# Performance work log

Measured on AMD Instinct MI355X. Metric: run time of the kernel, lower is better.

The kernel has to match this reference:

```python
import jax, jax.numpy as jnp
import numpy as np

MUL = 32            # multiplicity of 0e and 1o irreps
IN_DIM = MUL * 4    # 32 scalars + 32 vectors = 128
SH_DIM = 4          # 1x0e + 1x1o
N_EDGE_FEAT = 128
HIDDEN = 128
W_NUMEL = 4 * MUL * MUL  # 4 CG paths, uvw weights 32x1x32 each
EPS = 1e-5
INV_SQRT3 = 1.0 / np.sqrt(3.0)
PATH_NORM = 1.0 / np.sqrt(2.0 * MUL)  # 2 paths per output irrep, fan-in MUL


def _fc(edge_attr, W1, b1, W2, b2):
    h = jax.nn.relu(edge_attr @ W1 + b1)
    return h @ W2 + b2  # [E, W_NUMEL]


def _tensor_product(x, sh, w):
    # FullyConnectedTensorProduct for (32x0e+32x1o) x (1x0e+1x1o) -> (32x0e+32x1o)
    # CG (real w3j): 0x0->0: 1 ; 0x1->1, 1x0->1, 1x1->0: delta/sqrt(3)
    E = x.shape[0]
    x0 = x[:, :MUL]                      # [E,32]   scalars
    x1 = x[:, MUL:].reshape(E, MUL, 3)   # [E,32,3] vectors
    sh0 = sh[:, 0]                       # [E]
    sh1 = sh[:, 1:4]                     # [E,3]
    wA = w[:, 0 * MUL * MUL:1 * MUL * MUL].reshape(E, MUL, MUL)  # 0e x 0e -> 0e
    wB = w[:, 1 * MUL * MUL:2 * MUL * MUL].reshape(E, MUL, MUL)  # 0e x 1o -> 1o
    wC = w[:, 2 * MUL * MUL:3 * MUL * MUL].reshape(E, MUL, MUL)  # 1o x 0e -> 1o
    wD = w[:, 3 * MUL * MUL:4 * MUL * MUL].reshape(E, MUL, MUL)  # 1o x 1o -> 0e
    out0 = PATH_NORM * (
        jnp.einsum('eu,euw->ew', x0 * sh0[:, None], wA)
        + INV_SQRT3 * jnp.einsum('eui,ei,euw->ew', x1, sh1, wD))
    out1 = PATH_NORM * INV_SQRT3 * (
        jnp.einsum('eu,ei,euw->ewi', x0, sh1, wB)
        + jnp.einsum('eui,euw->ewi', x1 * sh0[:, None, None], wC))
    return jnp.concatenate([out0, out1.reshape(E, MUL * 3)], axis=-1)  # [E,128]


def _batch_norm(x, bn_weight, bn_bias):
    # e3nn-style equivariant BatchNorm (training stats): scalars get mean/var
    # normalization + affine; vectors get norm normalization + scale.
    N = x.shape[0]
    s = x[:, :MUL]                       # [N,32]
    v = x[:, MUL:].reshape(N, MUL, 3)    # [N,32,3]
    s = s - s.mean(axis=0)
    s = s * (jax.lax.rsqrt((s ** 2).mean(axis=0) + EPS) * bn_weight[:MUL]) + bn_bias
    v_norm = jax.lax.rsqrt((v ** 2).mean(axis=-1).mean(axis=0) + EPS)  # [32]
    v = v * (v_norm * bn_weight[MUL:])[None, :, None]
    return jnp.concatenate([s, v.reshape(N, MUL * 3)], axis=-1)


def _forward(node_attr, edge_index, edge_attr, edge_sh,
             W1, b1, W2, b2, bn_weight, bn_bias):
    edge_src, edge_dst = edge_index[0], edge_index[1]
    N = node_attr.shape[0]
    w = _fc(edge_attr, W1, b1, W2, b2)                     # [E, 4096]
    tp = _tensor_product(node_attr[edge_dst], edge_sh, w)  # [E, 128]
    # scatter mean over edge_src
    summed = jax.ops.segment_sum(tp, edge_src, num_segments=N)
    counts = jax.ops.segment_sum(jnp.ones((tp.shape[0],), tp.dtype), edge_src,
                                 num_segments=N)
    out = summed / jnp.maximum(counts, 1.0)[:, None]
    out = out + node_attr                                  # residual (same dim, pad=0)
    return _batch_norm(out, bn_weight, bn_bias)


def setup_inputs() -> dict:
    key = jax.random.key(0)
    ks = jax.random.split(key, 10)
    N, E = 10000, 60000
    node_attr = jax.random.normal(ks[0], (N, IN_DIM), jnp.float32)
    edge_index = jax.random.randint(ks[1], (2, E), 0, N)
    edge_attr = jax.random.normal(ks[2], (E, N_EDGE_FEAT), jnp.float32)
    edge_sh = jax.random.normal(ks[3], (E, SH_DIM), jnp.float32)
    W1 = jax.random.normal(ks[4], (N_EDGE_FEAT, HIDDEN), jnp.float32) / np.sqrt(N_EDGE_FEAT)
    b1 = jnp.zeros((HIDDEN,), jnp.float32)
    W2 = jax.random.normal(ks[5], (HIDDEN, W_NUMEL), jnp.float32) / np.sqrt(HIDDEN)
    b2 = jnp.zeros((W_NUMEL,), jnp.float32)
    bn_weight = jnp.ones((2 * MUL,), jnp.float32)
    bn_bias = jnp.zeros((MUL,), jnp.float32)
    return {"node_attr": node_attr, "edge_index": edge_index,
            "edge_attr": edge_attr, "edge_sh": edge_sh,
            "W1": W1, "b1": b1, "W2": W2, "b2": b2,
            "bn_weight": bn_weight, "bn_bias": bn_bias}


def reference(node_attr, edge_index, edge_attr, edge_sh,
              W1, b1, W2, b2, bn_weight, bn_bias):
    return _forward(node_attr, edge_index, edge_attr, edge_sh,
                    W1, b1, W2, b2, bn_weight, bn_bias)
```

## Files before the change

kernel.cpp:

```cpp
#include <hip/hip_runtime.h>
#include <math.h>

#define EPSV 1e-5f
#define IS3  0.57735026918962576f
#define PNRM 0.125f

typedef __attribute__((ext_vector_type(8)))  short  short8;
typedef __attribute__((ext_vector_type(16))) float  floatx16;

static __device__ inline unsigned short f2bf(float f) {
    unsigned int u = __float_as_uint(f);
    return (unsigned short)((u + 0x7fff + ((u >> 16) & 1)) >> 16);
}
static __device__ inline float bflo(unsigned int u) { return __uint_as_float(u << 16); }
static __device__ inline float bfhi(unsigned int u) { return __uint_as_float(u & 0xffff0000u); }

#define GLD16(gp, lp) __builtin_amdgcn_global_load_lds( \
    (const __attribute__((address_space(1))) unsigned int*)(gp), \
    (__attribute__((address_space(3))) unsigned int*)(lp), 16, 0, 0)

__global__ __launch_bounds__(256) void k0_sw(const float* __restrict__ src,
                                             unsigned short* __restrict__ dst,
                                             int total, int ncShift, int ncMask) {
    int i = blockIdx.x * 256 + threadIdx.x;
    if (i >= total) return;
    int k = i >> ncShift, c = i & ncMask;
    dst[(size_t)(c >> 5) * 4096 + (k >> 3) * 256 + (c & 31) * 8 + (k & 7)] = f2bf(src[i]);
}

__global__ __launch_bounds__(256) void k1_fc(const float* __restrict__ ea,
                                             const unsigned short* __restrict__ W1T,
                                             const float* __restrict__ b1,
                                             const int* __restrict__ ei,
                                             unsigned short* __restrict__ h,
                                             int* __restrict__ deg, int E) {
    __shared__ __align__(16) unsigned short W1s[16384];
    const int tid = threadIdx.x, lane = tid & 63, wv = tid >> 6;
    const int half = lane >> 5, col = lane & 31;
    const int e0 = blockIdx.x * 128;

    if (tid < 128) { int e = e0 + tid; if (e < E) atomicAdd(&deg[ei[e]], 1); }

#pragma unroll
    for (int q = 0; q < 8; ++q) {
        int chunk = wv * 8 + q;
        GLD16((const char*)W1T + chunk * 1024 + lane * 16, (char*)W1s + chunk * 1024);
    }

    int e = e0 + wv * 32 + col; if (e >= E) e = E - 1;
    short8 afr[8];
#pragma unroll
    for (int c = 0; c < 8; ++c) {
        const float4* p = (const float4*)(ea + (size_t)e * 128 + c * 16 + half * 8);
        float4 f0 = p[0], f1 = p[1];
        short8 v;
        v[0] = (short)f2bf(f0.x); v[1] = (short)f2bf(f0.y);
        v[2] = (short)f2bf(f0.z); v[3] = (short)f2bf(f0.w);
        v[4] = (short)f2bf(f1.x); v[5] = (short)f2bf(f1.y);
        v[6] = (short)f2bf(f1.z); v[7] = (short)f2bf(f1.w);
        afr[c] = v;
    }
    __syncthreads();

#pragma unroll
    for (int jt = 0; jt < 4; ++jt) {
        floatx16 d = {0,0,0,0,0,0,0,0,0,0,0,0,0,0,0,0};
#pragma unroll
        for (int c = 0; c < 8; ++c) {
            short8 bf = *(const short8*)((const char*)W1s + jt * 8192 + (2 * c + half) * 512 + col * 16);
            d = __builtin_amdgcn_mfma_f32_32x32x16_bf16(afr[c], bf, d, 0, 0, 0);
        }
        int j = jt * 32 + col;
        float b1v = b1[j];
#pragma unroll
        for (int reg = 0; reg < 16; ++reg) {
            int r = (reg & 3) + 8 * (reg >> 2) + 4 * half;
            int er = e0 + wv * 32 + r;
            if (er < E) {
                float v = d[reg] + b1v;
                v = v > 0.f ? v : 0.f;
                h[(size_t)er * 128 + j] = f2bf(v);
            }
        }
    }
}

__global__ __launch_bounds__(256, 2) void k2_mfma(const unsigned short* __restrict__ h,
                                                  const unsigned short* __restrict__ W2T,
                                                  const float* __restrict__ b2,
                                                  const float* __restrict__ na,
                                                  const int* __restrict__ ei,
                                                  const float* __restrict__ sh,
                                                  float* __restrict__ tp, int E) {
    __shared__ __align__(16) char smem[74752];
    unsigned short* As  = (unsigned short*)smem;
    unsigned short* Bs0 = (unsigned short*)(smem + 16384);
    unsigned short* Bs1 = (unsigned short*)(smem + 32768);
    unsigned short* Ctb = (unsigned short*)(smem + 49152);
    float* shs = (float*)(smem + 73728);
    float* red = (float*)smem;

    const int tid = threadIdx.x, lane = tid & 63, wv = tid >> 6;
    const int half = lane >> 5, col = lane & 31;
    const int ust = wv >> 1, esub = wv & 1;
    const int e0 = blockIdx.x * 64;

    if (tid < 64) {
        int e = e0 + tid; int ec = e < E ? e : E - 1;
        float4 s = *(const float4*)(sh + (size_t)ec * 4);
        *(float4*)&shs[tid * 4] = s;
    }

    for (int idx = tid; idx < 2048; idx += 256) {
        int el = idx & 63, u = idx >> 6;
        int e = e0 + el; int ec = e < E ? e : E - 1;
        int dn = ei[E + ec];
        const float* nar = na + (size_t)dn * 128;
        float x0  = nar[u];
        float x10 = nar[32 + u * 3], x11 = nar[33 + u * 3], x12 = nar[34 + u * 3];
        const float* shr = sh + (size_t)ec * 4;
        float s0 = shr[0], s1 = shr[1], s2 = shr[2], s3 = shr[3];
        int o = u * 64 + el;
        Ctb[0 * 2048 + o] = f2bf(x0 * s0);
        Ctb[1 * 2048 + o] = f2bf(x0);
        Ctb[2 * 2048 + o] = f2bf(x10);
        Ctb[3 * 2048 + o] = f2bf(x11);
        Ctb[4 * 2048 + o] = f2bf(x12);
        Ctb[5 * 2048 + o] = f2bf(IS3 * (x10 * s1 + x11 * s2 + x12 * s3));
    }

#pragma unroll
    for (int q = 0; q < 4; ++q) {
        int t = wv * 4 + q;
        int g = t >> 3;
        int jj = (t & 7) * 64 + lane;
        int e = e0 + g * 32 + (jj & 31); int ec = e < E ? e : E - 1;
        GLD16((const char*)h + (size_t)ec * 256 + (jj >> 5) * 16,
              (char*)As + g * 8192 + (t & 7) * 1024);
    }
#pragma unroll
    for (int q = 0; q < 4; ++q) {
        int chunk = wv * 4 + q;
        GLD16((const char*)W2T + chunk * 1024 + lane * 16, (char*)Bs0 + chunk * 1024);
    }
    __syncthreads();

    short8 afr[8];
#pragma unroll
    for (int c = 0; c < 8; ++c)
        afr[c] = *(const short8*)((const char*)As + esub * 8192 + (2 * c + half) * 512 + col * 16);

    float acc0[16] = {}, accB[16] = {}, accC0[16] = {}, accC1[16] = {}, accC2[16] = {};

    for (int p = 0; p < 64; ++p) {
        if (p < 63) {
            char* dst = ((p + 1) & 1) ? (char*)Bs1 : (char*)Bs0;
#pragma unroll
            for (int q = 0; q < 4; ++q) {
                int chunk = wv * 4 + q;
                GLD16((const char*)W2T + (p + 1) * 16384 + chunk * 1024 + lane * 16,
                      dst + chunk * 1024);
            }
        }
        const int ct = 2 * p + ust;
        const int b = ct >> 5, u = ct & 31;
        const char* bb = ((p & 1) ? (const char*)Bs1 : (const char*)Bs0) + ust * 8192;

        floatx16 d = {0,0,0,0,0,0,0,0,0,0,0,0,0,0,0,0};
#pragma unroll
        for (int c = 0; c < 8; ++c) {
            short8 bf = *(const short8*)(bb + (2 * c + half) * 512 + col * 16);
            d = __builtin_amdgcn_mfma_f32_32x32x16_bf16(afr[c], bf, d, 0, 0, 0);
        }
        float b2v = b2[ct * 32 + col];

        const int elb0 = esub * 32 + half * 4;
        if (b == 0 || b == 3) {
            const unsigned short* tb = Ctb + (b == 0 ? 0 : 5) * 2048;
#pragma unroll
            for (int q = 0; q < 4; ++q) {
                uint2 cv = *(const uint2*)&tb[u * 64 + elb0 + q * 8];
                acc0[q * 4 + 0] += bflo(cv.x) * (d[q * 4 + 0] + b2v);
                acc0[q * 4 + 1] += bfhi(cv.x) * (d[q * 4 + 1] + b2v);
                acc0[q * 4 + 2] += bflo(cv.y) * (d[q * 4 + 2] + b2v);
                acc0[q * 4 + 3] += bfhi(cv.y) * (d[q * 4 + 3] + b2v);
            }
        } else if (b == 1) {
#pragma unroll
            for (int q = 0; q < 4; ++q) {
                uint2 cv = *(const uint2*)&Ctb[1 * 2048 + u * 64 + elb0 + q * 8];
                accB[q * 4 + 0] += bflo(cv.x) * (d[q * 4 + 0] + b2v);
                accB[q * 4 + 1] += bfhi(cv.x) * (d[q * 4 + 1] + b2v);
                accB[q * 4 + 2] += bflo(cv.y) * (d[q * 4 + 2] + b2v);
                accB[q * 4 + 3] += bfhi(cv.y) * (d[q * 4 + 3] + b2v);
            }
        } else {
#pragma unroll
            for (int q = 0; q < 4; ++q) {
                uint2 c0 = *(const uint2*)&Ctb[2 * 2048 + u * 64 + elb0 + q * 8];
                uint2 c1 = *(const uint2*)&Ctb[3 * 2048 + u * 64 + elb0 + q * 8];
                uint2 c2 = *(const uint2*)&Ctb[4 * 2048 + u * 64 + elb0 + q * 8];
#pragma unroll
                for (int rr = 0; rr < 4; ++rr) {
                    float v = d[q * 4 + rr] + b2v;
                    float f0 = (rr == 0) ? bflo(c0.x) : (rr == 1) ? bfhi(c0.x) : (rr == 2) ? bflo(c0.y) : bfhi(c0.y);
                    float f1 = (rr == 0) ? bflo(c1.x) : (rr == 1) ? bfhi(c1.x) : (rr == 2) ? bflo(c1.y) : bfhi(c1.y);
                    float f2 = (rr == 0) ? bflo(c2.x) : (rr == 1) ? bfhi(c2.x) : (rr == 2) ? bflo(c2.y) : bfhi(c2.y);
                    accC0[q * 4 + rr] += f0 * v;
                    accC1[q * 4 + rr] += f1 * v;
                    accC2[q * 4 + rr] += f2 * v;
                }
            }
        }
        __syncthreads();
    }

    if (ust == 1) {
#pragma unroll
        for (int reg = 0; reg < 16; ++reg) {
            red[(((esub * 5 + 0) * 16 + reg) << 6) + lane] = acc0[reg];
            red[(((esub * 5 + 1) * 16 + reg) << 6) + lane] = accB[reg];
            red[(((esub * 5 + 2) * 16 + reg) << 6) + lane] = accC0[reg];
            red[(((esub * 5 + 3) * 16 + reg) << 6) + lane] = accC1[reg];
            red[(((esub * 5 + 4) * 16 + reg) << 6) + lane] = accC2[reg];
        }
    }
    __syncthreads();
    if (ust == 0) {
#pragma unroll
        for (int q = 0; q < 4; ++q) {
#pragma unroll
            for (int rr = 0; rr < 4; ++rr) {
                int reg = q * 4 + rr;
                int el = esub * 32 + q * 8 + half * 4 + rr;
                int e = e0 + el;
                if (e >= E) continue;
                float a0 = acc0[reg] + red[(((esub * 5 + 0) * 16 + reg) << 6) + lane];
                float aB = accB[reg] + red[(((esub * 5 + 1) * 16 + reg) << 6) + lane];
                float c0v = accC0[reg] + red[(((esub * 5 + 2) * 16 + reg) << 6) + lane];
                float c1v = accC1[reg] + red[(((esub * 5 + 3) * 16 + reg) << 6) + lane];
                float c2v = accC2[reg] + red[(((esub * 5 + 4) * 16 + reg) << 6) + lane];
                float4 sv = *(const float4*)&shs[el * 4];
                float* tpe = tp + (size_t)e * 128;
                tpe[col] = PNRM * a0;
                tpe[32 + col * 3 + 0] = PNRM * IS3 * (sv.y * aB + sv.x * c0v);
                tpe[32 + col * 3 + 1] = PNRM * IS3 * (sv.z * aB + sv.x * c1v);
                tpe[32 + col * 3 + 2] = PNRM * IS3 * (sv.w * aB + sv.x * c2v);
            }
        }
    }
}

__global__ __launch_bounds__(1024) void k_scan(const int* __restrict__ deg,
                                               int* __restrict__ rowptr, int N) {
    __shared__ int part[1024];
    const int tid = threadIdx.x;
    const int chunk = (N + 1023) / 1024;
    const int base = tid * chunk;
    int s = 0;
    for (int i = 0; i < chunk; ++i) {
        int n = base + i;
        if (n < N) s += deg[n];
    }
    part[tid] = s;
    __syncthreads();
    for (int off = 1; off < 1024; off <<= 1) {
        int t = 0;
        if (tid >= off) t = part[tid - off];
        __syncthreads();
        if (tid >= off) part[tid] += t;
        __syncthreads();
    }
    int prefix = (tid == 0) ? 0 : part[tid - 1];
    for (int i = 0; i < chunk; ++i) {
        int n = base + i;
        if (n < N) { rowptr[n] = prefix; prefix += deg[n]; }
    }
    if (tid == 0) rowptr[N] = part[1023];
}

__global__ __launch_bounds__(256) void k_fill(const int* __restrict__ ei,
                                              const int* __restrict__ rowptr,
                                              int* __restrict__ cursor,
                                              int* __restrict__ elist, int E) {
    int e = blockIdx.x * 256 + threadIdx.x;
    if (e >= E) return;
    int s = ei[e];
    int pos = rowptr[s] + atomicAdd(&cursor[s], 1);
    elist[pos] = e;
}

__global__ __launch_bounds__(256) void k4_gather(const float* __restrict__ tp,
                                                 const int* __restrict__ rowptr,
                                                 const int* __restrict__ elist,
                                                 const float* __restrict__ na,
                                                 float* __restrict__ pre,
                                                 float* __restrict__ stats, int N) {
    __shared__ float bns[96];
    const int tid = threadIdx.x;
    if (tid < 96) bns[tid] = 0.f;
    __syncthreads();
    const int o = tid & 127, hf = tid >> 7;
    for (int n = blockIdx.x * 2 + hf; n < N; n += gridDim.x * 2) {
        int r0 = rowptr[n], r1 = rowptr[n + 1];
        float s = 0.f;
        for (int j = r0; j < r1; ++j)
            s += tp[(size_t)elist[j] * 128 + o];
        int dg = r1 - r0;
        float cf = (float)(dg > 0 ? dg : 1);
        float v = s / cf + na[(size_t)n * 128 + o];
        pre[(size_t)n * 128 + o] = v;
        if (o < 32) {
            atomicAdd(&bns[o], v);
            atomicAdd(&bns[32 + o], v * v);
        } else {
            atomicAdd(&bns[64 + (o - 32) / 3], v * v);
        }
    }
    __syncthreads();
    if (tid < 96) atomicAdd(&stats[tid], bns[tid]);
}

__global__ __launch_bounds__(256) void k5_bn(const float* __restrict__ pre,
                                             const float* __restrict__ stats,
                                             const float* __restrict__ bnw,
                                             const float* __restrict__ bnb,
                                             float* __restrict__ out, int N) {
    size_t idx = (size_t)blockIdx.x * 256 + threadIdx.x;
    if (idx >= (size_t)N * 128) return;
    int o = (int)(idx & 127);
    float v = pre[idx];
    float invN = 1.f / (float)N;
    if (o < 32) {
        float m   = stats[o] * invN;
        float var = stats[32 + o] * invN - m * m;
        out[idx] = (v - m) * rsqrtf(var + EPSV) * bnw[o] + bnb[o];
    } else {
        int j = (o - 32) / 3;
        float vn = rsqrtf(stats[64 + j] * invN * (1.f / 3.f) + EPSV);
        out[idx] = v * vn * bnw[32 + j];
    }
}

extern "C" void kernel_launch(void* const* d_in, const int* in_sizes, int n_in,
                              void* d_out, int out_size, void* d_ws, size_t ws_size,
                              hipStream_t stream) {
    const float* node_attr  = (const float*)d_in[0];
    const int*   edge_index = (const int*)d_in[1];
    const float* edge_attr  = (const float*)d_in[2];
    const float* edge_sh    = (const float*)d_in[3];
    const float* W1  = (const float*)d_in[4];
    const float* b1  = (const float*)d_in[5];
    const float* W2  = (const float*)d_in[6];
    const float* b2  = (const float*)d_in[7];
    const float* bnw = (const float*)d_in[8];
    const float* bnb = (const float*)d_in[9];

    const int N = in_sizes[0] / 128;
    const int E = in_sizes[1] / 2;

    float* tp     = (float*)d_ws;
    float* pre    = tp + (size_t)E * 128;
    float* stats  = pre + (size_t)N * 128;
    int*   deg    = (int*)(stats + 96);
    int*   cursor = deg + N;
    int*   rowptr = cursor + N;
    int*   elist  = rowptr + N + 1;
    char* pbase = (char*)(elist + E);
    pbase += (16 - ((size_t)pbase & 15)) & 15;
    unsigned short* h   = (unsigned short*)pbase;
    unsigned short* W2T = h + (size_t)E * 128;
    unsigned short* W1T = W2T + (size_t)524288;

    hipMemsetAsync(stats, 0, (96 + 2 * (size_t)N) * sizeof(int), stream);

    k0_sw<<<(128 * 4096 + 255) / 256, 256, 0, stream>>>(W2, W2T, 128 * 4096, 12, 4095);
    k0_sw<<<(128 * 128 + 255) / 256, 256, 0, stream>>>(W1, W1T, 128 * 128, 7, 127);
    k1_fc<<<(E + 127) / 128, 256, 0, stream>>>(edge_attr, W1T, b1, edge_index, h, deg, E);
    k_scan<<<1, 1024, 0, stream>>>(deg, rowptr, N);
    k_fill<<<(E + 255) / 256, 256, 0, stream>>>(edge_index, rowptr, cursor, elist, E);
    k2_mfma<<<(E + 63) / 64, 256, 0, stream>>>(h, W2T, b2, node_attr, edge_index,
                                               edge_sh, tp, E);
    k4_gather<<<256, 256, 0, stream>>>(tp, rowptr, elist, node_attr, pre, stats, N);
    size_t ntot = (size_t)N * 128;
    k5_bn<<<(int)((ntot + 255) / 256), 256, 0, stream>>>(pre, stats, bnw, bnb,
                                                         (float*)d_out, N);
}
```

Before: 317.4 us.

## Triple-buffer W2 tiles, pre-swizzle hidden activations, fold scales, merge weight prep kernels

Several changes at once. The k2 W2 tile loads now use a three-slot ring with explicit vmcnt waits and raw barriers instead of double buffering with a full __syncthreads each iteration. k1 writes h in an MFMA-fragment order through an LDS bounce buffer, so k2 loads its A fragments straight from global memory. Normalisation constants and sh0 are folded into the LDS coefficient tables, and the sh-weighted combination is applied before the cross-wave reduction, which shrinks the reduction buffer. The two weight-swizzle launches are merged into one, and the gather kernel now launches twice as many blocks. The main risks are correctness of the hand-written waitcnt counts and the extra bf16 rounding from applying scales before conversion.

```diff
diff --git a/kernel.cpp b/kernel.cpp
--- a/kernel.cpp
+++ b/kernel.cpp
@@ -19,22 +19,33 @@
     (const __attribute__((address_space(1))) unsigned int*)(gp), \
     (__attribute__((address_space(3))) unsigned int*)(lp), 16, 0, 0)
 
-__global__ __launch_bounds__(256) void k0_sw(const float* __restrict__ src,
-                                             unsigned short* __restrict__ dst,
-                                             int total, int ncShift, int ncMask) {
+__global__ __launch_bounds__(256) void k0_sw(const float* __restrict__ W2,
+                                             const float* __restrict__ W1,
+                                             unsigned short* __restrict__ W2T,
+                                             unsigned short* __restrict__ W1T) {
     int i = blockIdx.x * 256 + threadIdx.x;
-    if (i >= total) return;
-    int k = i >> ncShift, c = i & ncMask;
-    dst[(size_t)(c >> 5) * 4096 + (k >> 3) * 256 + (c & 31) * 8 + (k & 7)] = f2bf(src[i]);
+    if (i < 524288) {
+        int tile = i >> 12, t = i & 4095;
+        int k = ((t >> 8) << 3) | (t & 7);
+        int c = (tile << 5) | ((t >> 3) & 31);
+        W2T[i] = f2bf(W2[(size_t)k * 4096 + c]);
+    } else if (i < 540672) {
+        int j = i - 524288;
+        int tile = j >> 12, t = j & 4095;
+        int k = ((t >> 8) << 3) | (t & 7);
+        int c = (tile << 5) | ((t >> 3) & 31);
+        W1T[j] = f2bf(W1[(size_t)k * 128 + c]);
+    }
 }
 
 __global__ __launch_bounds__(256) void k1_fc(const float* __restrict__ ea,
                                              const unsigned short* __restrict__ W1T,
                                              const float* __restrict__ b1,
                                              const int* __restrict__ ei,
-                                             unsigned short* __restrict__ h,
+                                             unsigned short* __restrict__ hsw,
                                              int* __restrict__ deg, int E) {
     __shared__ __align__(16) unsigned short W1s[16384];
+    __shared__ __align__(16) unsigned short bounce[4 * 1056];
     const int tid = threadIdx.x, lane = tid & 63, wv = tid >> 6;
     const int half = lane >> 5, col = lane & 31;
     const int e0 = blockIdx.x * 128;
@@ -62,6 +73,8 @@
     }
     __syncthreads();
 
+    unsigned short* myb = bounce + wv * 1056;
+    const int gg = blockIdx.x * 4 + wv;
 #pragma unroll
     for (int jt = 0; jt < 4; ++jt) {
         floatx16 d = {0,0,0,0,0,0,0,0,0,0,0,0,0,0,0,0};
@@ -70,46 +83,37 @@
             short8 bf = *(const short8*)((const char*)W1s + jt * 8192 + (2 * c + half) * 512 + col * 16);
             d = __builtin_amdgcn_mfma_f32_32x32x16_bf16(afr[c], bf, d, 0, 0, 0);
         }
-        int j = jt * 32 + col;
-        float b1v = b1[j];
+        float b1v = b1[jt * 32 + col];
 #pragma unroll
         for (int reg = 0; reg < 16; ++reg) {
             int r = (reg & 3) + 8 * (reg >> 2) + 4 * half;
-            int er = e0 + wv * 32 + r;
-            if (er < E) {
-                float v = d[reg] + b1v;
-                v = v > 0.f ? v : 0.f;
-                h[(size_t)er * 128 + j] = f2bf(v);
-            }
-        }
-    }
-}
-
-__global__ __launch_bounds__(256, 2) void k2_mfma(const unsigned short* __restrict__ h,
+            float v = d[reg] + b1v;
+            v = v > 0.f ? v : 0.f;
+            myb[(col >> 3) * 264 + r * 8 + (col & 7)] = f2bf(v);
+        }
+#pragma unroll
+        for (int s = 0; s < 2; ++s) {
+            short8 v = *(const short8*)&myb[(s * 2 + (lane >> 5)) * 264 + (lane & 31) * 8];
+            *(short8*)(hsw + (size_t)gg * 4096 + jt * 1024 + s * 512 + lane * 8) = v;
+        }
+    }
+}
+
+__global__ __launch_bounds__(256, 2) void k2_mfma(const unsigned short* __restrict__ hsw,
                                                   const unsigned short* __restrict__ W2T,
                                                   const float* __restrict__ b2,
                                                   const float* __restrict__ na,
                                                   const int* __restrict__ ei,
                                                   const float* __restrict__ sh,
                                                   float* __restrict__ tp, int E) {
-    __shared__ __align__(16) char smem[74752];
-    unsigned short* As  = (unsigned short*)smem;
-    unsigned short* Bs0 = (unsigned short*)(smem + 16384);
-    unsigned short* Bs1 = (unsigned short*)(smem + 32768);
+    __shared__ __align__(16) char smem[73728];
     unsigned short* Ctb = (unsigned short*)(smem + 49152);
-    float* shs = (float*)(smem + 73728);
     float* red = (float*)smem;
 
     const int tid = threadIdx.x, lane = tid & 63, wv = tid >> 6;
     const int half = lane >> 5, col = lane & 31;
     const int ust = wv >> 1, esub = wv & 1;
     const int e0 = blockIdx.x * 64;
-
-    if (tid < 64) {
-        int e = e0 + tid; int ec = e < E ? e : E - 1;
-        float4 s = *(const float4*)(sh + (size_t)ec * 4);
-        *(float4*)&shs[tid * 4] = s;
-    }
 
     for (int idx = tid; idx < 2048; idx += 256) {
         int el = idx & 63, u = idx >> 6;
@@ -121,50 +125,49 @@
         const float* shr = sh + (size_t)ec * 4;
         float s0 = shr[0], s1 = shr[1], s2 = shr[2], s3 = shr[3];
         int o = u * 64 + el;
-        Ctb[0 * 2048 + o] = f2bf(x0 * s0);
-        Ctb[1 * 2048 + o] = f2bf(x0);
-        Ctb[2 * 2048 + o] = f2bf(x10);
-        Ctb[3 * 2048 + o] = f2bf(x11);
-        Ctb[4 * 2048 + o] = f2bf(x12);
-        Ctb[5 * 2048 + o] = f2bf(IS3 * (x10 * s1 + x11 * s2 + x12 * s3));
-    }
-
-#pragma unroll
-    for (int q = 0; q < 4; ++q) {
-        int t = wv * 4 + q;
-        int g = t >> 3;
-        int jj = (t & 7) * 64 + lane;
-        int e = e0 + g * 32 + (jj & 31); int ec = e < E ? e : E - 1;
-        GLD16((const char*)h + (size_t)ec * 256 + (jj >> 5) * 16,
-              (char*)As + g * 8192 + (t & 7) * 1024);
-    }
+        Ctb[0 * 2048 + o] = f2bf(PNRM * x0 * s0);
+        Ctb[1 * 2048 + o] = f2bf(PNRM * IS3 * x0);
+        Ctb[2 * 2048 + o] = f2bf(PNRM * IS3 * s0 * x10);
+        Ctb[3 * 2048 + o] = f2bf(PNRM * IS3 * s0 * x11);
+        Ctb[4 * 2048 + o] = f2bf(PNRM * IS3 * s0 * x12);
+        Ctb[5 * 2048 + o] = f2bf(PNRM * IS3 * (x10 * s1 + x11 * s2 + x12 * s3));
+    }
+
+    const int gg = blockIdx.x * 2 + esub;
+    short8 afr[8];
+#pragma unroll
+    for (int c = 0; c < 8; ++c)
+        afr[c] = *(const short8*)(hsw + (size_t)gg * 4096 + (2 * c + half) * 256 + col * 8);
+
+    __syncthreads();
+
+    int offA = 0, offB = 16384, offC = 32768;
 #pragma unroll
     for (int q = 0; q < 4; ++q) {
         int chunk = wv * 4 + q;
-        GLD16((const char*)W2T + chunk * 1024 + lane * 16, (char*)Bs0 + chunk * 1024);
-    }
-    __syncthreads();
-
-    short8 afr[8];
-#pragma unroll
-    for (int c = 0; c < 8; ++c)
-        afr[c] = *(const short8*)((const char*)As + esub * 8192 + (2 * c + half) * 512 + col * 16);
+        GLD16((const char*)W2T + chunk * 1024 + lane * 16, smem + offA + chunk * 1024);
+    }
+    float b2cur = b2[ust * 32 + col];
+    asm volatile("" ::: "memory");
+#pragma unroll
+    for (int q = 0; q < 4; ++q) {
+        int chunk = wv * 4 + q;
+        GLD16((const char*)W2T + 16384 + chunk * 1024 + lane * 16, smem + offB + chunk * 1024);
+    }
+    float b2nxt = b2[(2 + ust) * 32 + col];
+    asm volatile("" ::: "memory");
 
     float acc0[16] = {}, accB[16] = {}, accC0[16] = {}, accC1[16] = {}, accC2[16] = {};
+    const int elb0 = esub * 32 + half * 4;
 
     for (int p = 0; p < 64; ++p) {
-        if (p < 63) {
-            char* dst = ((p + 1) & 1) ? (char*)Bs1 : (char*)Bs0;
-#pragma unroll
-            for (int q = 0; q < 4; ++q) {
-                int chunk = wv * 4 + q;
-                GLD16((const char*)W2T + (p + 1) * 16384 + chunk * 1024 + lane * 16,
-                      dst + chunk * 1024);
-            }
-        }
+        if (p == 63) asm volatile("s_waitcnt vmcnt(0)" ::: "memory");
+        else         asm volatile("s_waitcnt vmcnt(5)" ::: "memory");
+        asm volatile("s_barrier" ::: "memory");
+
         const int ct = 2 * p + ust;
         const int b = ct >> 5, u = ct & 31;
-        const char* bb = ((p & 1) ? (const char*)Bs1 : (const char*)Bs0) + ust * 8192;
+        const char* bb = smem + offA + ust * 8192;
 
         floatx16 d = {0,0,0,0,0,0,0,0,0,0,0,0,0,0,0,0};
 #pragma unroll
@@ -172,9 +175,8 @@
             short8 bf = *(const short8*)(bb + (2 * c + half) * 512 + col * 16);
             d = __builtin_amdgcn_mfma_f32_32x32x16_bf16(afr[c], bf, d, 0, 0, 0);
         }
-        float b2v = b2[ct * 32 + col];
-
-        const int elb0 = esub * 32 + half * 4;
+        const float b2v = b2cur;
+
         if (b == 0 || b == 3) {
             const unsigned short* tb = Ctb + (b == 0 ? 0 : 5) * 2048;
 #pragma unroll
@@ -197,32 +199,51 @@
         } else {
 #pragma unroll
             for (int q = 0; q < 4; ++q) {
-                uint2 c0 = *(const uint2*)&Ctb[2 * 2048 + u * 64 + elb0 + q * 8];
-                uint2 c1 = *(const uint2*)&Ctb[3 * 2048 + u * 64 + elb0 + q * 8];
-                uint2 c2 = *(const uint2*)&Ctb[4 * 2048 + u * 64 + elb0 + q * 8];
+                uint2 cu0 = *(const uint2*)&Ctb[2 * 2048 + u * 64 + elb0 + q * 8];
+                uint2 cu1 = *(const uint2*)&Ctb[3 * 2048 + u * 64 + elb0 + q * 8];
+                uint2 cu2 = *(const uint2*)&Ctb[4 * 2048 + u * 64 + elb0 + q * 8];
+                float f0[4] = {bflo(cu0.x), bfhi(cu0.x), bflo(cu0.y), bfhi(cu0.y)};
+                float f1[4] = {bflo(cu1.x), bfhi(cu1.x), bflo(cu1.y), bfhi(cu1.y)};
+                float f2[4] = {bflo(cu2.x), bfhi(cu2.x), bflo(cu2.y), bfhi(cu2.y)};
 #pragma unroll
                 for (int rr = 0; rr < 4; ++rr) {
                     float v = d[q * 4 + rr] + b2v;
-                    float f0 = (rr == 0) ? bflo(c0.x) : (rr == 1) ? bfhi(c0.x) : (rr == 2) ? bflo(c0.y) : bfhi(c0.y);
-                    float f1 = (rr == 0) ? bflo(c1.x) : (rr == 1) ? bfhi(c1.x) : (rr == 2) ? bflo(c1.y) : bfhi(c1.y);
-                    float f2 = (rr == 0) ? bflo(c2.x) : (rr == 1) ? bfhi(c2.x) : (rr == 2) ? bflo(c2.y) : bfhi(c2.y);
-                    accC0[q * 4 + rr] += f0 * v;
-                    accC1[q * 4 + rr] += f1 * v;
-                    accC2[q * 4 + rr] += f2 * v;
+                    accC0[q * 4 + rr] += f0[rr] * v;
+                    accC1[q * 4 + rr] += f1[rr] * v;
+                    accC2[q * 4 + rr] += f2[rr] * v;
                 }
             }
         }
-        __syncthreads();
-    }
-
+
+        float b2new = 0.f;
+        if (p + 2 < 64) {
+#pragma unroll
+            for (int q = 0; q < 4; ++q) {
+                int chunk = wv * 4 + q;
+                GLD16((const char*)W2T + (p + 2) * 16384 + chunk * 1024 + lane * 16,
+                      smem + offC + chunk * 1024);
+            }
+            b2new = b2[(2 * (p + 2) + ust) * 32 + col];
+        }
+        int t = offA; offA = offB; offB = offC; offC = t;
+        b2cur = b2nxt; b2nxt = b2new;
+    }
+
+    __syncthreads();
     if (ust == 1) {
 #pragma unroll
-        for (int reg = 0; reg < 16; ++reg) {
-            red[(((esub * 5 + 0) * 16 + reg) << 6) + lane] = acc0[reg];
-            red[(((esub * 5 + 1) * 16 + reg) << 6) + lane] = accB[reg];
-            red[(((esub * 5 + 2) * 16 + reg) << 6) + lane] = accC0[reg];
-            red[(((esub * 5 + 3) * 16 + reg) << 6) + lane] = accC1[reg];
-            red[(((esub * 5 + 4) * 16 + reg) << 6) + lane] = accC2[reg];
+        for (int q = 0; q < 4; ++q) {
+#pragma unroll
+            for (int rr = 0; rr < 4; ++rr) {
+                int reg = q * 4 + rr;
+                int el = esub * 32 + q * 8 + half * 4 + rr;
+                int e = e0 + el; int ec = e < E ? e : E - 1;
+                float4 sv = *(const float4*)(sh + (size_t)ec * 4);
+                red[(((esub * 4 + 0) * 16 + reg) << 6) + lane] = acc0[reg];
+                red[(((esub * 4 + 1) * 16 + reg) << 6) + lane] = sv.y * accB[reg] + accC0[reg];
+                red[(((esub * 4 + 2) * 16 + reg) << 6) + lane] = sv.z * accB[reg] + accC1[reg];
+                red[(((esub * 4 + 3) * 16 + reg) << 6) + lane] = sv.w * accB[reg] + accC2[reg];
+            }
         }
     }
     __syncthreads();
@@ -235,17 +256,16 @@
                 int el = esub * 32 + q * 8 + half * 4 + rr;
                 int e = e0 + el;
                 if (e >= E) continue;
-                float a0 = acc0[reg] + red[(((esub * 5 + 0) * 16 + reg) << 6) + lane];
-                float aB = accB[reg] + red[(((esub * 5 + 1) * 16 + reg) << 6) + lane];
-                float c0v = accC0[reg] + red[(((esub * 5 + 2) * 16 + reg) << 6) + lane];
-                float c1v = accC1[reg] + red[(((esub * 5 + 3) * 16 + reg) << 6) + lane];
-                float c2v = accC2[reg] + red[(((esub * 5 + 4) * 16 + reg) << 6) + lane];
-                float4 sv = *(const float4*)&shs[el * 4];
+                float4 sv = *(const float4*)(sh + (size_t)e * 4);
+                float a0 = acc0[reg] + red[(((esub * 4 + 0) * 16 + reg) << 6) + lane];
+                float o0 = sv.y * accB[reg] + accC0[reg] + red[(((esub * 4 + 1) * 16 + reg) << 6) + lane];
+                float o1 = sv.z * accB[reg] + accC1[reg] + red[(((esub * 4 + 2) * 16 + reg) << 6) + lane];
+                float o2 = sv.w * accB[reg] + accC2[reg] + red[(((esub * 4 + 3) * 16 + reg) << 6) + lane];
                 float* tpe = tp + (size_t)e * 128;
-                tpe[col] = PNRM * a0;
-                tpe[32 + col * 3 + 0] = PNRM * IS3 * (sv.y * aB + sv.x * c0v);
-                tpe[32 + col * 3 + 1] = PNRM * IS3 * (sv.z * aB + sv.x * c1v);
-                tpe[32 + col * 3 + 2] = PNRM * IS3 * (sv.w * aB + sv.x * c2v);
+                tpe[col] = a0;
+                tpe[32 + col * 3 + 0] = o0;
+                tpe[32 + col * 3 + 1] = o1;
+                tpe[32 + col * 3 + 2] = o2;
             }
         }
     }
@@ -358,6 +378,7 @@
 
     const int N = in_sizes[0] / 128;
     const int E = in_sizes[1] / 2;
+    const int ngroups = ((E + 127) / 128) * 4;
 
     float* tp     = (float*)d_ws;
     float* pre    = tp + (size_t)E * 128;
@@ -368,20 +389,19 @@
     int*   elist  = rowptr + N + 1;
     char* pbase = (char*)(elist + E);
     pbase += (16 - ((size_t)pbase & 15)) & 15;
-    unsigned short* h   = (unsigned short*)pbase;
-    unsigned short* W2T = h + (size_t)E * 128;
+    unsigned short* hsw = (unsigned short*)pbase;
+    unsigned short* W2T = hsw + (size_t)ngroups * 4096;
     unsigned short* W1T = W2T + (size_t)524288;
 
     hipMemsetAsync(stats, 0, (96 + 2 * (size_t)N) * sizeof(int), stream);
 
-    k0_sw<<<(128 * 4096 + 255) / 256, 256, 0, stream>>>(W2, W2T, 128 * 4096, 12, 4095);
-    k0_sw<<<(128 * 128 + 255) / 256, 256, 0, stream>>>(W1, W1T, 128 * 128, 7, 127);
-    k1_fc<<<(E + 127) / 128, 256, 0, stream>>>(edge_attr, W1T, b1, edge_index, h, deg, E);
+    k0_sw<<<(540672 + 255) / 256, 256, 0, stream>>>(W2, W1, W2T, W1T);
+    k1_fc<<<(E + 127) / 128, 256, 0, stream>>>(edge_attr, W1T, b1, edge_index, hsw, deg, E);
     k_scan<<<1, 1024, 0, stream>>>(deg, rowptr, N);
     k_fill<<<(E + 255) / 256, 256, 0, stream>>>(edge_index, rowptr, cursor, elist, E);
-    k2_mfma<<<(E + 63) / 64, 256, 0, stream>>>(h, W2T, b2, node_attr, edge_index,
+    k2_mfma<<<(E + 63) / 64, 256, 0, stream>>>(hsw, W2T, b2, node_attr, edge_index,
                                                edge_sh, tp, E);
-    k4_gather<<<256, 256, 0, stream>>>(tp, rowptr, elist, node_attr, pre, stats, N);
+    k4_gather<<<512, 256, 0, stream>>>(tp, rowptr, elist, node_attr, pre, stats, N);
     size_t ntot = (size_t)N * 128;
     k5_bn<<<(int)((ntot + 255) / 256), 256, 0, stream>>>(pre, stats, bnw, bnb,
                                                          (float*)d_out, N);
```

Result: faster. 300.7 us (-5.3%).
